# Kernel tuning notes

Measured on AMD Instinct MI355X. Metric: run time of the kernel, lower is better.

The kernel has to match this reference:

```python
import jax, jax.numpy as jnp
import numpy as np

DIM = 768
HEADS = 8
HEAD_DIM = DIM // HEADS  # 96, divisible by 6 for 3-axis RoPE
ROPE_BASE = 10000.0


def rotary_pe_3d(x, coords):
    """Apply 3D-coordinate rotary embedding.
    x: [B, h, L, d] with d % 6 == 0; coords: [B, L, 3].
    Head dim is split into 3 equal blocks, one per spatial axis; each block
    gets rotate-half RoPE with angle = coord_axis * inv_freq.
    """
    B, h, L, d = x.shape
    d3 = d // 3
    half = d3 // 2
    inv_freq = 1.0 / (ROPE_BASE ** (jnp.arange(half, dtype=x.dtype) / half))  # [half]
    ang = coords[..., None] * inv_freq  # [B, L, 3, half]
    cos = jnp.cos(ang)[:, None]  # [B, 1, L, 3, half]
    sin = jnp.sin(ang)[:, None]
    xr = x.reshape(B, h, L, 3, d3)
    x1, x2 = xr[..., :half], xr[..., half:]
    out = jnp.concatenate([x1 * cos - x2 * sin, x1 * sin + x2 * cos], axis=-1)
    return out.reshape(B, h, L, d)


def setup_inputs() -> dict:
    key = jax.random.key(0)
    ks = jax.random.split(key, 9)
    B, Lq, Lk = 2, 2048, 2048
    s = DIM ** -0.5
    return {
        "Q_in": jax.random.normal(ks[0], (B, Lq, DIM), jnp.float32),
        "K_in": jax.random.normal(ks[1], (B, Lk, DIM), jnp.float32),
        "V_in": jax.random.normal(ks[2], (B, Lk, DIM), jnp.float32),
        "coords_q": jax.random.uniform(ks[3], (B, Lq, 3), jnp.float32) * 10.0,
        "coords_k": jax.random.uniform(ks[4], (B, Lk, 3), jnp.float32) * 10.0,
        "Wq": jax.random.normal(ks[5], (DIM, DIM), jnp.float32) * s,
        "Wk": jax.random.normal(ks[6], (DIM, DIM), jnp.float32) * s,
        "Wv": jax.random.normal(ks[7], (DIM, DIM), jnp.float32) * s,
        "Wo": jax.random.normal(ks[8], (DIM, DIM), jnp.float32) * s,
    }


def _split_heads(x, h):
    B, L, C = x.shape
    return x.reshape(B, L, h, C // h).transpose(0, 2, 1, 3)  # [B,h,L,d]


def reference(Q_in, K_in, V_in, coords_q, coords_k, Wq, Wk, Wv, Wo):
    scale = HEAD_DIM ** -0.5
    q = _split_heads(Q_in @ Wq.T, HEADS)
    k = _split_heads(K_in @ Wk.T, HEADS)
    v = _split_heads(V_in @ Wv.T, HEADS)
    q = rotary_pe_3d(q, coords_q)
    k = rotary_pe_3d(k, coords_k)
    attn = jnp.einsum('bhqd,bhkd->bhqk', q, k) * scale
    attn = jax.nn.softmax(attn, axis=-1)
    out = jnp.einsum('bhqk,bhkd->bhqd', attn, v)
    B, h, L, d = out.shape
    out = out.transpose(0, 2, 1, 3).reshape(B, L, h * d)
    return out @ Wo.T
```

## Files before the change

### kernel.cpp

```cpp
#include <hip/hip_runtime.h>
#include <stdint.h>

#define H 8
#define DH 96
#define L 2048
#define NB 2
#define D 768

typedef unsigned short u16;
typedef unsigned int u32;
typedef __attribute__((ext_vector_type(8))) __bf16 bf16x8;
typedef __attribute__((ext_vector_type(4))) float f32x4;
typedef __attribute__((ext_vector_type(4))) u32 u32x4;
typedef __attribute__((ext_vector_type(2))) u32 u32x2;
typedef __attribute__((ext_vector_type(4))) u16 u16x4;

#define QSCALE 0.14724444f

static __device__ __forceinline__ u16 f2bf(float f) {
  union { __bf16 h; u16 u; } v;
  v.h = (__bf16)f;
  return v.u;
}

static __device__ __forceinline__ bf16x8 cvt8r(f32x4 a, f32x4 b) {
  bf16x8 r;
  r[0] = (__bf16)a[0]; r[1] = (__bf16)a[1]; r[2] = (__bf16)a[2]; r[3] = (__bf16)a[3];
  r[4] = (__bf16)b[0]; r[5] = (__bf16)b[1]; r[6] = (__bf16)b[2]; r[7] = (__bf16)b[3];
  return r;
}

__global__ __launch_bounds__(256, 3)
void proj_qkv(const float* __restrict__ Qin, const float* __restrict__ Kin,
              const float* __restrict__ Vin,
              const float* __restrict__ Wq, const float* __restrict__ Wk,
              const float* __restrict__ Wv,
              const float* __restrict__ cq, const float* __restrict__ ck,
              u16* __restrict__ qo, u16* __restrict__ ko, u16* __restrict__ vo)
{
  __shared__ u16 a_lds[2][64 * 40];
  __shared__ u16 b_lds[2][192 * 40];
  const int tid = threadIdx.x;
  const int lane = tid & 63;
  const int w = tid >> 6;
  const int wr = w >> 1, wc = w & 1;
  const int fr = lane & 15;
  const int hi = lane >> 4;

  const int f = blockIdx.x;
  const int xcd = f & 7;
  const int g = f >> 3;
  const int bx = g & 3;
  const int h2 = g >> 2;
  const int byp = h2 & 7;
  const int z = h2 >> 3;
  const int by = xcd + 8 * byp;
  const int row0 = by * 64;
  const int col0 = bx * 192;

  const float* A = (z == 0) ? Qin : ((z == 1) ? Kin : Vin);
  const float* W = (z == 0) ? Wq : ((z == 1) ? Wk : Wv);

  const int arow = tid >> 2;
  const int acol = (tid & 3) * 8;
  const float* pA = A + (size_t)(row0 + arow) * D + acol;
  const float* pB0 = W + (size_t)(col0 + arow) * D + acol;
  const float* pB1 = pB0 + (size_t)64 * D;
  const float* pB2 = pB0 + (size_t)128 * D;

  f32x4 acc[2][6] = {};
  f32x4 Ra[2], Rb[6];

  auto issue = [&](int k) {
    Ra[0] = *(const f32x4*)(pA + k);
    Ra[1] = *(const f32x4*)(pA + k + 4);
    Rb[0] = *(const f32x4*)(pB0 + k);
    Rb[1] = *(const f32x4*)(pB0 + k + 4);
    Rb[2] = *(const f32x4*)(pB1 + k);
    Rb[3] = *(const f32x4*)(pB1 + k + 4);
    Rb[4] = *(const f32x4*)(pB2 + k);
    Rb[5] = *(const f32x4*)(pB2 + k + 4);
  };
  auto stage = [&](int bi) {
    *(bf16x8*)(&a_lds[bi][arow * 40 + acol]) = cvt8r(Ra[0], Ra[1]);
    *(bf16x8*)(&b_lds[bi][arow * 40 + acol]) = cvt8r(Rb[0], Rb[1]);
    *(bf16x8*)(&b_lds[bi][(arow + 64) * 40 + acol]) = cvt8r(Rb[2], Rb[3]);
    *(bf16x8*)(&b_lds[bi][(arow + 128) * 40 + acol]) = cvt8r(Rb[4], Rb[5]);
  };
  auto compute = [&](int bi) {
    bf16x8 af[2], bf[6];
#pragma unroll
    for (int m = 0; m < 2; m++)
      af[m] = *(const bf16x8*)(&a_lds[bi][(wr * 32 + m * 16 + fr) * 40 + hi * 8]);
#pragma unroll
    for (int n = 0; n < 6; n++)
      bf[n] = *(const bf16x8*)(&b_lds[bi][(wc * 96 + n * 16 + fr) * 40 + hi * 8]);
#pragma unroll
    for (int m = 0; m < 2; m++)
#pragma unroll
      for (int n = 0; n < 6; n++)
        acc[m][n] = __builtin_amdgcn_mfma_f32_16x16x32_bf16(af[m], bf[n], acc[m][n], 0, 0, 0);
  };

  issue(0);
  stage(0);
  __syncthreads();

  int cur = 0;
#pragma unroll 1
  for (int t = 0; t < 24; t++) {
    if (t + 1 < 24) issue((t + 1) * 32);
    compute(cur);
    if (t + 1 < 24) stage(cur ^ 1);
    __syncthreads();
    cur ^= 1;
  }

  const int hh = (col0 + wc * 96) / DH;
  if (z == 2) {
#pragma unroll
    for (int m = 0; m < 2; m++) {
      int rbase = row0 + wr * 32 + m * 16 + hi * 4;
#pragma unroll
      for (int n = 0; n < 6; n++) {
        int dd = n * 16 + fr;
#pragma unroll
        for (int r = 0; r < 4; r++) {
          int row = rbase + r;
          int b = row >> 11, l = row & (L - 1);
          vo[((size_t)((b * H + hh) * DH + dd)) * L + l] = f2bf(acc[m][n][r]);
        }
      }
    }
  } else {
    const float* coords = (z == 0) ? cq : ck;
    u16* outp = (z == 0) ? qo : ko;
    const float postscale = (z == 0) ? QSCALE : 1.0f;
    const float invf = exp2f(-(float)fr * 0.83048202372184058f);
#pragma unroll
    for (int m = 0; m < 2; m++) {
      int rbase = row0 + wr * 32 + m * 16 + hi * 4;
#pragma unroll
      for (int np = 0; np < 3; np++) {
        int n1 = np * 2;
        int dd1 = n1 * 16 + fr;
#pragma unroll
        for (int r = 0; r < 4; r++) {
          int row = rbase + r;
          int b = row >> 11, l = row & (L - 1);
          float coord = coords[((size_t)(b * L + l)) * 3 + np];
          float ang = coord * invf;
          float sn = __sinf(ang), cs = __cosf(ang);
          float x1 = acc[m][n1][r], x2 = acc[m][n1 + 1][r];
          size_t base = ((size_t)((b * H + hh) * L + l)) * DH;
          outp[base + dd1] = f2bf((x1 * cs - x2 * sn) * postscale);
          outp[base + dd1 + 16] = f2bf((x1 * sn + x2 * cs) * postscale);
        }
      }
    }
  }
}

#define KSTR 104
#define VSTR 72
#define NT   (L / 64)
__global__ __launch_bounds__(256, 2)
void attn_fwd(const u16* __restrict__ q_ws, const u16* __restrict__ k_ws,
              const u16* __restrict__ vt_ws, u16* __restrict__ ao)
{
  __shared__ u16 k_lds[2][64 * KSTR];
  __shared__ u16 vt_lds[2][96 * VSTR];
  const int tid = threadIdx.x;
  const int lane = tid & 63;
  const int w = tid >> 6;

  const int f = blockIdx.x;
  const int xr = f & 7;
  const int g = f >> 3;
  const int qx = g & 31;
  const int bh = xr + 8 * (g >> 5);
  const int q0 = qx * 64;

  const int fr = lane & 15;
  const int hi = lane >> 4;
  const int fko = hi * 8;

  int kg_off[3], kl_off[3], vg_off[3], vl0_off[3], vl1_off[3];
#pragma unroll
  for (int it = 0; it < 3; it++) {
    int ch = tid + it * 256;
    int krow = ch / 12, koff = (ch % 12) * 8;
    kg_off[it] = krow * DH + koff;
    kl_off[it] = krow * KSTR + koff;
    int vrow = ch >> 3, vq = (ch & 7) * 2;
    vg_off[it] = vrow * L + vq * 4;
    int s0 = ((vq >> 3) << 5) | ((vq & 3) << 3) | (((vq >> 2) & 1) << 2);
    int vq1 = vq + 1;
    int s1 = ((vq1 >> 3) << 5) | ((vq1 & 3) << 3) | (((vq1 >> 2) & 1) << 2);
    vl0_off[it] = vrow * VSTR + s0;
    vl1_off[it] = vrow * VSTR + s1;
  }

  bf16x8 qf[3];
  const u16* qbase = q_ws + ((size_t)bh * L + q0 + w * 16 + fr) * DH;
#pragma unroll
  for (int ks = 0; ks < 3; ks++)
    qf[ks] = *(const bf16x8*)(qbase + ks * 32 + fko);

  f32x4 o[6] = {};
  float m_r = -1e30f, l_r = 0.f;

  const u16* kbase = k_ws + (size_t)bh * L * DH;
  const u16* vtbase = vt_ws + (size_t)bh * DH * L;

  u32x4 kreg[3], vreg[3];
#pragma unroll
  for (int it = 0; it < 3; it++) {
    kreg[it] = *(const u32x4*)(kbase + kg_off[it]);
    vreg[it] = *(const u32x4*)(vtbase + vg_off[it]);
  }
#pragma unroll
  for (int it = 0; it < 3; it++) {
    *(u32x4*)(&k_lds[0][kl_off[it]]) = kreg[it];
    u32x2 lo = { vreg[it][0], vreg[it][1] };
    u32x2 hi2 = { vreg[it][2], vreg[it][3] };
    *(u32x2*)(&vt_lds[0][vl0_off[it]]) = lo;
    *(u32x2*)(&vt_lds[0][vl1_off[it]]) = hi2;
  }
  __syncthreads();

  int cur = 0;
  for (int t = 0; t < NT; t++) {
    if (t + 1 < NT) {
      const u16* kb = kbase + (size_t)(t + 1) * 64 * DH;
      const u16* vb = vtbase + (t + 1) * 64;
#pragma unroll
      for (int it = 0; it < 3; it++) {
        kreg[it] = *(const u32x4*)(kb + kg_off[it]);
        vreg[it] = *(const u32x4*)(vb + vg_off[it]);
      }
    }

    f32x4 s[4] = {};
#pragma unroll
    for (int ks = 0; ks < 3; ks++)
#pragma unroll
      for (int kf = 0; kf < 4; kf++) {
        bf16x8 kfrag = *(const bf16x8*)(&k_lds[cur][(kf * 16 + fr) * KSTR + ks * 32 + fko]);
        s[kf] = __builtin_amdgcn_mfma_f32_16x16x32_bf16(kfrag, qf[ks], s[kf], 0, 0, 0);
      }

    float pmax = fmaxf(fmaxf(s[0][0], s[0][1]), fmaxf(s[0][2], s[0][3]));
#pragma unroll
    for (int kf = 1; kf < 4; kf++)
      pmax = fmaxf(pmax, fmaxf(fmaxf(s[kf][0], s[kf][1]), fmaxf(s[kf][2], s[kf][3])));
    if (!__all(pmax - m_r <= 8.0f)) {
      float mx = fmaxf(pmax, __shfl_xor(pmax, 16));
      mx = fmaxf(mx, __shfl_xor(mx, 32));
      float mn = fmaxf(m_r, mx);
      float alpha = exp2f(m_r - mn);
      m_r = mn;
      l_r *= alpha;
#pragma unroll
      for (int df = 0; df < 6; df++)
#pragma unroll
        for (int r = 0; r < 4; r++)
          o[df][r] *= alpha;
    }

    float p[4][4];
    float rs = 0.f;
#pragma unroll
    for (int kf = 0; kf < 4; kf++)
#pragma unroll
      for (int r = 0; r < 4; r++) {
        float pv = exp2f(s[kf][r] - m_r);
        p[kf][r] = pv;
        rs += pv;
      }
    l_r += rs;

    bf16x8 pt[2];
#pragma unroll
    for (int ks = 0; ks < 2; ks++)
#pragma unroll
      for (int j = 0; j < 8; j++)
        pt[ks][j] = (__bf16)p[2 * ks + (j >> 2)][j & 3];

#pragma unroll
    for (int ks = 0; ks < 2; ks++)
#pragma unroll
      for (int df = 0; df < 6; df++) {
        bf16x8 vfrag = *(const bf16x8*)(&vt_lds[cur][(df * 16 + fr) * VSTR + ks * 32 + fko]);
        o[df] = __builtin_amdgcn_mfma_f32_16x16x32_bf16(vfrag, pt[ks], o[df], 0, 0, 0);
      }

    if (t + 1 < NT) {
#pragma unroll
      for (int it = 0; it < 3; it++) {
        *(u32x4*)(&k_lds[cur ^ 1][kl_off[it]]) = kreg[it];
        u32x2 lo = { vreg[it][0], vreg[it][1] };
        u32x2 hi2 = { vreg[it][2], vreg[it][3] };
        *(u32x2*)(&vt_lds[cur ^ 1][vl0_off[it]]) = lo;
        *(u32x2*)(&vt_lds[cur ^ 1][vl1_off[it]]) = hi2;
      }
      __syncthreads();
      cur ^= 1;
    }
  }

  float l_tot = l_r + __shfl_xor(l_r, 16);
  l_tot += __shfl_xor(l_tot, 32);
  const int b = bh >> 3, hh = bh & 7;
  const int l = q0 + w * 16 + fr;
  const float inv = 1.f / l_tot;
  u16* aop = ao + ((size_t)(b * L + l)) * D + hh * DH + hi * 4;
#pragma unroll
  for (int df = 0; df < 6; df++) {
    u16x4 pk;
#pragma unroll
    for (int r = 0; r < 4; r++)
      pk[r] = f2bf(o[df][r] * inv);
    *(u16x4*)(aop + df * 16) = pk;
  }
}

__global__ __launch_bounds__(256, 2)
void gemm_out(const u16* __restrict__ A, const float* __restrict__ W,
              float* __restrict__ out)
{
  __shared__ u16 a_lds[2][64 * 40];
  __shared__ u16 b_lds[2][64 * 40];
  const int tid = threadIdx.x;
  const int lane = tid & 63;
  const int w = tid >> 6;
  const int wr = w >> 1, wc = w & 1;

  const int f = blockIdx.x;
  const int xr = f & 7;
  const int g = f >> 3;
  const int bx = g % 12;
  const int wq = g / 12;
  const int by = xr + 8 * wq;
  const int row0 = by * 64;
  const int col0 = bx * 64;

  f32x4 acc[2][2] = {};
  const int srow = tid >> 2;
  const int scol = (tid & 3) * 8;
  const u16* pA = A + (size_t)(row0 + srow) * D + scol;
  const float* pW = W + (size_t)(col0 + srow) * D + scol;
  const int fr = lane & 15;
  const int fk = (lane >> 4) * 8;

  auto issueG = [&](int k, u32x4* ra, f32x4* rb) {
    ra[0] = *(const u32x4*)(pA + k);
    rb[0] = *(const f32x4*)(pW + k);
    rb[1] = *(const f32x4*)(pW + k + 4);
  };
  auto writeG = [&](int bi, const u32x4* ra, const f32x4* rb) {
    *(u32x4*)(&a_lds[bi][srow * 40 + scol]) = ra[0];
    *(bf16x8*)(&b_lds[bi][srow * 40 + scol]) = cvt8r(rb[0], rb[1]);
  };
  auto computeG = [&](int bi) {
    bf16x8 af[2], bfr[2];
#pragma unroll
    for (int m = 0; m < 2; m++)
      af[m] = *(const bf16x8*)(&a_lds[bi][(wr * 32 + m * 16 + fr) * 40 + fk]);
#pragma unroll
    for (int n = 0; n < 2; n++)
      bfr[n] = *(const bf16x8*)(&b_lds[bi][(wc * 32 + n * 16 + fr) * 40 + fk]);
#pragma unroll
    for (int m = 0; m < 2; m++)
#pragma unroll
      for (int n = 0; n < 2; n++)
        acc[m][n] = __builtin_amdgcn_mfma_f32_16x16x32_bf16(af[m], bfr[n], acc[m][n], 0, 0, 0);
  };

  u32x4 raA[1], raB[1];
  f32x4 rbA[2], rbB[2];
  issueG(0, raB, rbB);
  writeG(0, raB, rbB);
  issueG(32, raA, rbA);
  __syncthreads();

  for (int k0 = 0; k0 < D; k0 += 64) {
    if (k0 + 64 < D) issueG(k0 + 64, raB, rbB);
    computeG(0);
    writeG(1, raA, rbA);
    __syncthreads();
    if (k0 + 96 < D) issueG(k0 + 96, raA, rbA);
    computeG(1);
    if (k0 + 64 < D) writeG(0, raB, rbB);
    __syncthreads();
  }

#pragma unroll
  for (int m = 0; m < 2; m++) {
    int rbase = row0 + wr * 32 + m * 16 + (lane >> 4) * 4;
#pragma unroll
    for (int n = 0; n < 2; n++) {
      int c = col0 + wc * 32 + n * 16 + fr;
#pragma unroll
      for (int r = 0; r < 4; r++)
        out[(size_t)(rbase + r) * D + c] = acc[m][n][r];
    }
  }
}

extern "C" void kernel_launch(void* const* d_in, const int* in_sizes, int n_in,
                              void* d_out, int out_size, void* d_ws, size_t ws_size,
                              hipStream_t stream) {
  (void)in_sizes; (void)n_in; (void)out_size;
  const float* Qin = (const float*)d_in[0];
  const float* Kin = (const float*)d_in[1];
  const float* Vin = (const float*)d_in[2];
  const float* cq  = (const float*)d_in[3];
  const float* ck  = (const float*)d_in[4];
  const float* Wq  = (const float*)d_in[5];
  const float* Wk  = (const float*)d_in[6];
  const float* Wv  = (const float*)d_in[7];
  const float* Wo  = (const float*)d_in[8];
  float* out = (float*)d_out;

  const size_t per = (size_t)NB * H * L * DH;
  if (ws_size < 4 * per * sizeof(u16)) return;

  u16* q_ws  = (u16*)d_ws;
  u16* k_ws  = q_ws + per;
  u16* vt_ws = k_ws + per;
  u16* ao_ws = vt_ws + per;

  proj_qkv<<<dim3(768), dim3(256), 0, stream>>>(
      Qin, Kin, Vin, Wq, Wk, Wv, cq, ck, q_ws, k_ws, vt_ws);
  attn_fwd<<<dim3(32 * NB * H), dim3(256), 0, stream>>>(q_ws, k_ws, vt_ws, ao_ws);
  gemm_out<<<dim3(12 * 64), dim3(256), 0, stream>>>(ao_ws, Wo, out);
}
```

Measured before the change: 101.8 us.

## Load K tiles via direct global-to-LDS DMA and drop K padding

The K tile in the attention kernel is now copied global-to-LDS with global_load_lds, which skips the register staging and explicit LDS stores. The K row stride shrinks from 104 to 96 so the contiguous DMA layout matches, which may bring back LDS bank conflicts on the K fragment reads. The row-max reduction is reshaped into a shallower tree, and the output GEMM's launch bounds are raised to target 3 blocks per SM. There is no explicit wait on the DMA (vmcnt) before the barrier, so correctness relies on the compiler or barrier semantics.

```diff
diff --git a/kernel.cpp b/kernel.cpp
--- a/kernel.cpp
+++ b/kernel.cpp
@@ -161,7 +161,7 @@
   }
 }
 
-#define KSTR 104
+#define KSTR 96
 #define VSTR 72
 #define NT   (L / 64)
 __global__ __launch_bounds__(256, 2)
@@ -185,13 +185,13 @@
   const int hi = lane >> 4;
   const int fko = hi * 8;
 
-  int kg_off[3], kl_off[3], vg_off[3], vl0_off[3], vl1_off[3];
+  const u16* kbase = k_ws + (size_t)bh * L * DH;
+  const u16* vtbase = vt_ws + (size_t)bh * DH * L;
+
+  int vg_off[3], vl0_off[3], vl1_off[3];
 #pragma unroll
   for (int it = 0; it < 3; it++) {
     int ch = tid + it * 256;
-    int krow = ch / 12, koff = (ch % 12) * 8;
-    kg_off[it] = krow * DH + koff;
-    kl_off[it] = krow * KSTR + koff;
     int vrow = ch >> 3, vq = (ch & 7) * 2;
     vg_off[it] = vrow * L + vq * 4;
     int s0 = ((vq >> 3) << 5) | ((vq & 3) << 3) | (((vq >> 2) & 1) << 2);
@@ -201,6 +201,17 @@
     vl1_off[it] = vrow * VSTR + s1;
   }
 
+  auto kdma = [&](int t, int bi) {
+#pragma unroll
+    for (int it = 0; it < 3; it++) {
+      const u16* gp = kbase + (size_t)t * 64 * DH + ((size_t)(tid + it * 256)) * 8;
+      u16* lp = &k_lds[bi][(size_t)(w * 64 + it * 256) * 8];
+      __builtin_amdgcn_global_load_lds(
+          (const __attribute__((address_space(1))) u32*)gp,
+          (__attribute__((address_space(3))) u32*)lp, 16, 0, 0);
+    }
+  };
+
   bf16x8 qf[3];
   const u16* qbase = q_ws + ((size_t)bh * L + q0 + w * 16 + fr) * DH;
 #pragma unroll
@@ -210,18 +221,13 @@
   f32x4 o[6] = {};
   float m_r = -1e30f, l_r = 0.f;
 
-  const u16* kbase = k_ws + (size_t)bh * L * DH;
-  const u16* vtbase = vt_ws + (size_t)bh * DH * L;
-
-  u32x4 kreg[3], vreg[3];
+  u32x4 vreg[3];
+  kdma(0, 0);
+#pragma unroll
+  for (int it = 0; it < 3; it++)
+    vreg[it] = *(const u32x4*)(vtbase + vg_off[it]);
 #pragma unroll
   for (int it = 0; it < 3; it++) {
-    kreg[it] = *(const u32x4*)(kbase + kg_off[it]);
-    vreg[it] = *(const u32x4*)(vtbase + vg_off[it]);
-  }
-#pragma unroll
-  for (int it = 0; it < 3; it++) {
-    *(u32x4*)(&k_lds[0][kl_off[it]]) = kreg[it];
     u32x2 lo = { vreg[it][0], vreg[it][1] };
     u32x2 hi2 = { vreg[it][2], vreg[it][3] };
     *(u32x2*)(&vt_lds[0][vl0_off[it]]) = lo;
@@ -232,13 +238,11 @@
   int cur = 0;
   for (int t = 0; t < NT; t++) {
     if (t + 1 < NT) {
-      const u16* kb = kbase + (size_t)(t + 1) * 64 * DH;
+      kdma(t + 1, cur ^ 1);
       const u16* vb = vtbase + (t + 1) * 64;
 #pragma unroll
-      for (int it = 0; it < 3; it++) {
-        kreg[it] = *(const u32x4*)(kb + kg_off[it]);
+      for (int it = 0; it < 3; it++)
         vreg[it] = *(const u32x4*)(vb + vg_off[it]);
-      }
     }
 
     f32x4 s[4] = {};
@@ -250,10 +254,12 @@
         s[kf] = __builtin_amdgcn_mfma_f32_16x16x32_bf16(kfrag, qf[ks], s[kf], 0, 0, 0);
       }
 
-    float pmax = fmaxf(fmaxf(s[0][0], s[0][1]), fmaxf(s[0][2], s[0][3]));
-#pragma unroll
-    for (int kf = 1; kf < 4; kf++)
-      pmax = fmaxf(pmax, fmaxf(fmaxf(s[kf][0], s[kf][1]), fmaxf(s[kf][2], s[kf][3])));
+    float a0 = fmaxf(fmaxf(s[0][0], s[0][1]), s[0][2]);
+    float a1 = fmaxf(fmaxf(s[0][3], s[1][0]), s[1][1]);
+    float a2 = fmaxf(fmaxf(s[1][2], s[1][3]), s[2][0]);
+    float a3 = fmaxf(fmaxf(s[2][1], s[2][2]), s[2][3]);
+    float a4 = fmaxf(fmaxf(s[3][0], s[3][1]), s[3][2]);
+    float pmax = fmaxf(fmaxf(fmaxf(a0, a1), a2), fmaxf(fmaxf(a3, a4), s[3][3]));
     if (!__all(pmax - m_r <= 8.0f)) {
       float mx = fmaxf(pmax, __shfl_xor(pmax, 16));
       mx = fmaxf(mx, __shfl_xor(mx, 32));
@@ -298,7 +304,6 @@
     if (t + 1 < NT) {
 #pragma unroll
       for (int it = 0; it < 3; it++) {
-        *(u32x4*)(&k_lds[cur ^ 1][kl_off[it]]) = kreg[it];
         u32x2 lo = { vreg[it][0], vreg[it][1] };
         u32x2 hi2 = { vreg[it][2], vreg[it][3] };
         *(u32x2*)(&vt_lds[cur ^ 1][vl0_off[it]]) = lo;
@@ -325,7 +330,7 @@
   }
 }
 
-__global__ __launch_bounds__(256, 2)
+__global__ __launch_bounds__(256, 3)
 void gemm_out(const u16* __restrict__ A, const float* __restrict__ W,
               float* __restrict__ out)
 {
```

Result: no change. 103.6 us (+1.7%).

## Switch attention to 32x32x16 MFMA with split-KV waves and LDS merge

Applied to the files above, without the earlier changes.

Rewrites the attention inner loop to use 32x32x16 bf16 MFMA tiles. Each pair of waves covers 32 query rows and splits each 64-key tile into two 32-key halves, keeping separate online-softmax state per wave. The two partial results are merged through LDS at the end. K and V LDS layouts are permuted to match the new fragment layout, and the V stride is padded. The aim is fewer MFMA issues and LDS fragment loads per FLOP, at the cost of an extra cross-wave reduction and sync. gemm_out's launch bound is also raised to 3 blocks per SM.

```diff
diff --git a/kernel.cpp b/kernel.cpp
--- a/kernel.cpp
+++ b/kernel.cpp
@@ -9,8 +9,10 @@
 
 typedef unsigned short u16;
 typedef unsigned int u32;
+typedef __attribute__((ext_vector_type(4))) __bf16 bf16x4;
 typedef __attribute__((ext_vector_type(8))) __bf16 bf16x8;
 typedef __attribute__((ext_vector_type(4))) float f32x4;
+typedef __attribute__((ext_vector_type(16))) float f32x16;
 typedef __attribute__((ext_vector_type(4))) u32 u32x4;
 typedef __attribute__((ext_vector_type(2))) u32 u32x2;
 typedef __attribute__((ext_vector_type(4))) u16 u16x4;
@@ -162,14 +164,14 @@
 }
 
 #define KSTR 104
-#define VSTR 72
+#define VSTR 76
 #define NT   (L / 64)
 __global__ __launch_bounds__(256, 2)
 void attn_fwd(const u16* __restrict__ q_ws, const u16* __restrict__ k_ws,
               const u16* __restrict__ vt_ws, u16* __restrict__ ao)
 {
-  __shared__ u16 k_lds[2][64 * KSTR];
-  __shared__ u16 vt_lds[2][96 * VSTR];
+  __shared__ __attribute__((aligned(16))) u16 k_lds[2][64 * KSTR];
+  __shared__ __attribute__((aligned(16))) u16 vt_lds[2][96 * VSTR];
   const int tid = threadIdx.x;
   const int lane = tid & 63;
   const int w = tid >> 6;
@@ -181,151 +183,182 @@
   const int bh = xr + 8 * (g >> 5);
   const int q0 = qx * 64;
 
-  const int fr = lane & 15;
-  const int hi = lane >> 4;
-  const int fko = hi * 8;
-
-  int kg_off[3], kl_off[3], vg_off[3], vl0_off[3], vl1_off[3];
+  const int qlo = lane & 31;
+  const int hi32 = lane >> 5;
+  const int wq = w >> 1;
+  const int kk0 = (w & 1) * 32;
+
+  const u16* kbase = k_ws + (size_t)bh * L * DH;
+  const u16* vtbase = vt_ws + (size_t)bh * DH * L;
+
+  const int perm[4] = {0, 2, 1, 3};
+
+  int kg_off[3], kl0[3], kl1[3];
+  int vg_off[3], vl0[3], vl1[3];
 #pragma unroll
   for (int it = 0; it < 3; it++) {
     int ch = tid + it * 256;
-    int krow = ch / 12, koff = (ch % 12) * 8;
-    kg_off[it] = krow * DH + koff;
-    kl_off[it] = krow * KSTR + koff;
+    int krow = ch / 12, dc = ch % 12;
+    kg_off[it] = krow * DH + dc * 8;
+    int c0 = dc * 2;
+    kl0[it] = krow * KSTR + (c0 >> 2) * 16 + perm[c0 & 3] * 4;
+    kl1[it] = krow * KSTR + (c0 >> 2) * 16 + perm[(c0 + 1) & 3] * 4;
     int vrow = ch >> 3, vq = (ch & 7) * 2;
     vg_off[it] = vrow * L + vq * 4;
-    int s0 = ((vq >> 3) << 5) | ((vq & 3) << 3) | (((vq >> 2) & 1) << 2);
-    int vq1 = vq + 1;
-    int s1 = ((vq1 >> 3) << 5) | ((vq1 & 3) << 3) | (((vq1 >> 2) & 1) << 2);
-    vl0_off[it] = vrow * VSTR + s0;
-    vl1_off[it] = vrow * VSTR + s1;
-  }
-
-  bf16x8 qf[3];
-  const u16* qbase = q_ws + ((size_t)bh * L + q0 + w * 16 + fr) * DH;
-#pragma unroll
-  for (int ks = 0; ks < 3; ks++)
-    qf[ks] = *(const bf16x8*)(qbase + ks * 32 + fko);
-
-  f32x4 o[6] = {};
+    vl0[it] = vrow * VSTR + (vq >> 2) * 16 + perm[vq & 3] * 4;
+    vl1[it] = vrow * VSTR + (vq >> 2) * 16 + perm[(vq + 1) & 3] * 4;
+  }
+
+  bf16x8 qf[6];
+  {
+    const u16* qb = q_ws + ((size_t)bh * L + q0 + wq * 32 + qlo) * DH;
+#pragma unroll
+    for (int s = 0; s < 6; s++) {
+      bf16x4 a = *(const bf16x4*)(qb + s * 16 + hi32 * 4);
+      bf16x4 b = *(const bf16x4*)(qb + s * 16 + hi32 * 4 + 8);
+      bf16x8 q;
+      q[0] = a[0]; q[1] = a[1]; q[2] = a[2]; q[3] = a[3];
+      q[4] = b[0]; q[5] = b[1]; q[6] = b[2]; q[7] = b[3];
+      qf[s] = q;
+    }
+  }
+
+  f32x16 o[3] = {};
   float m_r = -1e30f, l_r = 0.f;
 
-  const u16* kbase = k_ws + (size_t)bh * L * DH;
-  const u16* vtbase = vt_ws + (size_t)bh * DH * L;
-
   u32x4 kreg[3], vreg[3];
-#pragma unroll
-  for (int it = 0; it < 3; it++) {
-    kreg[it] = *(const u32x4*)(kbase + kg_off[it]);
-    vreg[it] = *(const u32x4*)(vtbase + vg_off[it]);
-  }
-#pragma unroll
-  for (int it = 0; it < 3; it++) {
-    *(u32x4*)(&k_lds[0][kl_off[it]]) = kreg[it];
-    u32x2 lo = { vreg[it][0], vreg[it][1] };
-    u32x2 hi2 = { vreg[it][2], vreg[it][3] };
-    *(u32x2*)(&vt_lds[0][vl0_off[it]]) = lo;
-    *(u32x2*)(&vt_lds[0][vl1_off[it]]) = hi2;
-  }
+  auto kissue = [&](int t) {
+    const u16* kb = kbase + (size_t)t * 64 * DH;
+    const u16* vb = vtbase + t * 64;
+#pragma unroll
+    for (int it = 0; it < 3; it++) {
+      kreg[it] = *(const u32x4*)(kb + kg_off[it]);
+      vreg[it] = *(const u32x4*)(vb + vg_off[it]);
+    }
+  };
+  auto kwrite = [&](int bi) {
+#pragma unroll
+    for (int it = 0; it < 3; it++) {
+      u32x2 klo = { kreg[it][0], kreg[it][1] };
+      u32x2 khi = { kreg[it][2], kreg[it][3] };
+      *(u32x2*)(&k_lds[bi][kl0[it]]) = klo;
+      *(u32x2*)(&k_lds[bi][kl1[it]]) = khi;
+      u32x2 vlo = { vreg[it][0], vreg[it][1] };
+      u32x2 vhi = { vreg[it][2], vreg[it][3] };
+      *(u32x2*)(&vt_lds[bi][vl0[it]]) = vlo;
+      *(u32x2*)(&vt_lds[bi][vl1[it]]) = vhi;
+    }
+  };
+
+  kissue(0);
+  kwrite(0);
   __syncthreads();
 
   int cur = 0;
   for (int t = 0; t < NT; t++) {
-    if (t + 1 < NT) {
-      const u16* kb = kbase + (size_t)(t + 1) * 64 * DH;
-      const u16* vb = vtbase + (t + 1) * 64;
-#pragma unroll
-      for (int it = 0; it < 3; it++) {
-        kreg[it] = *(const u32x4*)(kb + kg_off[it]);
-        vreg[it] = *(const u32x4*)(vb + vg_off[it]);
-      }
-    }
-
-    f32x4 s[4] = {};
-#pragma unroll
-    for (int ks = 0; ks < 3; ks++)
-#pragma unroll
-      for (int kf = 0; kf < 4; kf++) {
-        bf16x8 kfrag = *(const bf16x8*)(&k_lds[cur][(kf * 16 + fr) * KSTR + ks * 32 + fko]);
-        s[kf] = __builtin_amdgcn_mfma_f32_16x16x32_bf16(kfrag, qf[ks], s[kf], 0, 0, 0);
-      }
-
-    float pmax = fmaxf(fmaxf(s[0][0], s[0][1]), fmaxf(s[0][2], s[0][3]));
-#pragma unroll
-    for (int kf = 1; kf < 4; kf++)
-      pmax = fmaxf(pmax, fmaxf(fmaxf(s[kf][0], s[kf][1]), fmaxf(s[kf][2], s[kf][3])));
+    if (t + 1 < NT) kissue(t + 1);
+
+    f32x16 s2 = {};
+#pragma unroll
+    for (int s = 0; s < 6; s++) {
+      bf16x8 kfrag = *(const bf16x8*)(
+          &k_lds[cur][(kk0 + qlo) * KSTR + s * 16 + hi32 * 8]);
+      s2 = __builtin_amdgcn_mfma_f32_32x32x16_bf16(kfrag, qf[s], s2, 0, 0, 0);
+    }
+
+    float a0 = fmaxf(fmaxf(s2[0], s2[1]), s2[2]);
+    float a1 = fmaxf(fmaxf(s2[3], s2[4]), s2[5]);
+    float a2 = fmaxf(fmaxf(s2[6], s2[7]), s2[8]);
+    float a3 = fmaxf(fmaxf(s2[9], s2[10]), s2[11]);
+    float a4 = fmaxf(fmaxf(s2[12], s2[13]), s2[14]);
+    float pmax = fmaxf(fmaxf(fmaxf(a0, a1), a2), fmaxf(fmaxf(a3, a4), s2[15]));
     if (!__all(pmax - m_r <= 8.0f)) {
-      float mx = fmaxf(pmax, __shfl_xor(pmax, 16));
-      mx = fmaxf(mx, __shfl_xor(mx, 32));
+      float mx = fmaxf(pmax, __shfl_xor(pmax, 32));
       float mn = fmaxf(m_r, mx);
       float alpha = exp2f(m_r - mn);
       m_r = mn;
       l_r *= alpha;
 #pragma unroll
-      for (int df = 0; df < 6; df++)
-#pragma unroll
-        for (int r = 0; r < 4; r++)
-          o[df][r] *= alpha;
-    }
-
-    float p[4][4];
+      for (int db = 0; db < 3; db++)
+#pragma unroll
+        for (int r = 0; r < 16; r++)
+          o[db][r] *= alpha;
+    }
+
+    float p[16];
     float rs = 0.f;
 #pragma unroll
-    for (int kf = 0; kf < 4; kf++)
-#pragma unroll
-      for (int r = 0; r < 4; r++) {
-        float pv = exp2f(s[kf][r] - m_r);
-        p[kf][r] = pv;
-        rs += pv;
+    for (int r = 0; r < 16; r++) {
+      p[r] = exp2f(s2[r] - m_r);
+      rs += p[r];
+    }
+    l_r += rs;
+
+    bf16x8 pt[2];
+#pragma unroll
+    for (int s = 0; s < 2; s++)
+#pragma unroll
+      for (int j = 0; j < 8; j++)
+        pt[s][j] = (__bf16)p[s * 8 + j];
+
+#pragma unroll
+    for (int s = 0; s < 2; s++)
+#pragma unroll
+      for (int db = 0; db < 3; db++) {
+        bf16x8 vfrag = *(const bf16x8*)(
+            &vt_lds[cur][(db * 32 + qlo) * VSTR + kk0 + s * 16 + hi32 * 8]);
+        o[db] = __builtin_amdgcn_mfma_f32_32x32x16_bf16(vfrag, pt[s], o[db], 0, 0, 0);
       }
-    l_r += rs;
-
-    bf16x8 pt[2];
-#pragma unroll
-    for (int ks = 0; ks < 2; ks++)
-#pragma unroll
-      for (int j = 0; j < 8; j++)
-        pt[ks][j] = (__bf16)p[2 * ks + (j >> 2)][j & 3];
-
-#pragma unroll
-    for (int ks = 0; ks < 2; ks++)
-#pragma unroll
-      for (int df = 0; df < 6; df++) {
-        bf16x8 vfrag = *(const bf16x8*)(&vt_lds[cur][(df * 16 + fr) * VSTR + ks * 32 + fko]);
-        o[df] = __builtin_amdgcn_mfma_f32_16x16x32_bf16(vfrag, pt[ks], o[df], 0, 0, 0);
-      }
 
     if (t + 1 < NT) {
-#pragma unroll
-      for (int it = 0; it < 3; it++) {
-        *(u32x4*)(&k_lds[cur ^ 1][kl_off[it]]) = kreg[it];
-        u32x2 lo = { vreg[it][0], vreg[it][1] };
-        u32x2 hi2 = { vreg[it][2], vreg[it][3] };
-        *(u32x2*)(&vt_lds[cur ^ 1][vl0_off[it]]) = lo;
-        *(u32x2*)(&vt_lds[cur ^ 1][vl1_off[it]]) = hi2;
-      }
+      kwrite(cur ^ 1);
       __syncthreads();
       cur ^= 1;
     }
   }
 
-  float l_tot = l_r + __shfl_xor(l_r, 16);
-  l_tot += __shfl_xor(l_tot, 32);
-  const int b = bh >> 3, hh = bh & 7;
-  const int l = q0 + w * 16 + fr;
-  const float inv = 1.f / l_tot;
-  u16* aop = ao + ((size_t)(b * L + l)) * D + hh * DH + hi * 4;
-#pragma unroll
-  for (int df = 0; df < 6; df++) {
-    u16x4 pk;
-#pragma unroll
-    for (int r = 0; r < 4; r++)
-      pk[r] = f2bf(o[df][r] * inv);
-    *(u16x4*)(aop + df * 16) = pk;
-  }
-}
-
-__global__ __launch_bounds__(256, 2)
+  float l_w = l_r + __shfl_xor(l_r, 32);
+
+  {
+    float* xb = (float*)&k_lds[wq][0];
+    const int base = lane * 52;
+    if (w & 1) {
+#pragma unroll
+      for (int db = 0; db < 3; db++)
+#pragma unroll
+        for (int rg = 0; rg < 4; rg++) {
+          f32x4 v = { o[db][rg * 4], o[db][rg * 4 + 1],
+                      o[db][rg * 4 + 2], o[db][rg * 4 + 3] };
+          *(f32x4*)&xb[base + db * 16 + rg * 4] = v;
+        }
+      xb[base + 48] = m_r;
+      xb[base + 49] = l_w;
+    }
+    __syncthreads();
+    if (!(w & 1)) {
+      float m1 = xb[base + 48], l1 = xb[base + 49];
+      float ms = fmaxf(m_r, m1);
+      float c0 = exp2f(m_r - ms), c1 = exp2f(m1 - ms);
+      float inv = 1.f / (l_w * c0 + l1 * c1);
+      const int b = bh >> 3, hh = bh & 7;
+      const int lrow = q0 + wq * 32 + qlo;
+      u16* aop = ao + ((size_t)(b * L + lrow)) * D + hh * DH;
+#pragma unroll
+      for (int db = 0; db < 3; db++)
+#pragma unroll
+        for (int rg = 0; rg < 4; rg++) {
+          f32x4 op = *(const f32x4*)&xb[base + db * 16 + rg * 4];
+          u16x4 pk;
+#pragma unroll
+          for (int r4 = 0; r4 < 4; r4++)
+            pk[r4] = f2bf((o[db][rg * 4 + r4] * c0 + op[r4] * c1) * inv);
+          *(u16x4*)(aop + db * 32 + rg * 8 + hi32 * 4) = pk;
+        }
+    }
+  }
+}
+
+__global__ __launch_bounds__(256, 3)
 void gemm_out(const u16* __restrict__ A, const float* __restrict__ W,
               float* __restrict__ out)
 {
```

Result: faster. 99.09 us (-2.7%).
